# Performance work log

Hardware: AMD Instinct MI355X
Metric: run time of the kernel (lower is better)

Reference implementation:

```python
import jax, jax.numpy as jnp
import numpy as np

VIS_DIM = 768
LBL_DIM = 128
HID = 256
VIS_W = 0.4
LBL_W = 0.6
TEMP = 1.0
EPS = 1e-12  # torch F.normalize default eps


def setup_inputs() -> dict:
    key = jax.random.key(0)
    ks = jax.random.split(key, 8)
    B, N = 32, 4096
    visual_feats = jax.random.normal(ks[0], (B, N, VIS_DIM), dtype=jnp.float32)
    label_context = jax.random.normal(ks[1], (B, LBL_DIM), dtype=jnp.float32)
    visual_mask = jnp.ones((B, N), dtype=bool)
    # scorer MLP params (stored [in, out] for x @ W)
    W1 = jax.random.normal(ks[2], (VIS_DIM, HID), dtype=jnp.float32) / np.sqrt(VIS_DIM)
    b1 = jnp.zeros((HID,), dtype=jnp.float32)
    W2 = jax.random.normal(ks[3], (HID, 1), dtype=jnp.float32) / np.sqrt(HID)
    b2 = jnp.zeros((1,), dtype=jnp.float32)
    # label -> visual projection
    Wp = jax.random.normal(ks[4], (LBL_DIM, VIS_DIM), dtype=jnp.float32) / np.sqrt(LBL_DIM)
    bp = jnp.zeros((VIS_DIM,), dtype=jnp.float32)
    return {
        "visual_feats": visual_feats,
        "label_context": label_context,
        "W1": W1, "b1": b1, "W2": W2, "b2": b2, "Wp": Wp, "bp": bp,
        "visual_mask": visual_mask,
        "k": 192,
    }


def _l2norm(x):
    n = jnp.linalg.norm(x, axis=-1, keepdims=True)
    return x / jnp.maximum(n, EPS)


def reference(visual_feats, label_context, W1, b1, W2, b2, Wp, bp, visual_mask, k):
    B, N, D = visual_feats.shape
    # scoring MLP: [B,N,D] -> [B,N]
    h = jnp.maximum(jnp.einsum('bnd,dh->bnh', visual_feats, W1) + b1, 0.0)
    visual_scores = (jnp.einsum('bnh,ho->bno', h, W2) + b2)[..., 0]
    # label projection [B,D] then cosine similarity against each patch
    label_proj = label_context @ Wp + bp              # [B, D]
    vis_n = _l2norm(visual_feats)                     # [B, N, D]
    lbl_n = _l2norm(label_proj)[:, None, :]           # [B, 1, D]
    label_scores = jnp.sum(vis_n * lbl_n, axis=-1)    # [B, N]
    combined = (VIS_W * visual_scores + LBL_W * label_scores) / TEMP
    combined = jnp.where(visual_mask, combined, -jnp.inf)
    k = min(int(k), N)
    topk_scores, topk_indices = jax.lax.top_k(combined, k)   # [B, k]
    selected_feats = jnp.take_along_axis(visual_feats, topk_indices[..., None], axis=1)
    return selected_feats, topk_indices
```

## Files before the change

kernel.cpp:

```cpp
#include <hip/hip_runtime.h>
#include <hip/hip_bf16.h>

#define B_   32
#define N_   4096
#define D_   768
#define HID_ 256

#define SX 64.0f
#define SW 1024.0f
#define INV_S (1.0f / 65536.0f)

typedef unsigned long long ull;
typedef _Float16 half8 __attribute__((ext_vector_type(8)));
typedef _Float16 half4 __attribute__((ext_vector_type(4)));
typedef float f32x16 __attribute__((ext_vector_type(16)));

__device__ __forceinline__ void gload_lds16(const void* g, void* l) {
  __builtin_amdgcn_global_load_lds(
      (const __attribute__((address_space(1))) void*)g,
      (__attribute__((address_space(3))) void*)l, 16, 0, 0);
}

__global__ __launch_bounds__(256) void prep_kernel(
    const float* __restrict__ W1, _Float16* __restrict__ whi,
    _Float16* __restrict__ wlo, const float* __restrict__ lc,
    const float* __restrict__ Wp, const float* __restrict__ bp,
    float* __restrict__ lbl_n) {
  if (blockIdx.x < 96) {
    int c = blockIdx.x;
    int h = threadIdx.x;
    half8 vh, vl;
#pragma unroll
    for (int j = 0; j < 8; ++j) {
      float w = W1[(size_t)(c * 8 + j) * 256 + h] * SW;
      _Float16 hi = (_Float16)w;
      vh[j] = hi;
      vl[j] = (_Float16)(w - (float)hi);
    }
    *(half8*)&whi[((size_t)c * 256 + h) * 8] = vh;
    *(half8*)&wlo[((size_t)c * 256 + h) * 8] = vl;
    return;
  }
  int b = blockIdx.x - 96;
  int t = threadIdx.x;
  __shared__ float s_lc[128];
  __shared__ float s_out[768];
  __shared__ float s_red[4];

  if (t < 128) s_lc[t] = lc[b * 128 + t];
  __syncthreads();

  float sumsq = 0.f;
  for (int d = t; d < D_; d += 256) {
    float acc = bp[d];
    for (int k = 0; k < 128; ++k) acc += s_lc[k] * Wp[k * D_ + d];
    s_out[d] = acc;
    sumsq += acc * acc;
  }
  for (int off = 32; off >= 1; off >>= 1) sumsq += __shfl_xor(sumsq, off);
  if ((t & 63) == 0) s_red[t >> 6] = sumsq;
  __syncthreads();
  float tot = s_red[0] + s_red[1] + s_red[2] + s_red[3];
  float inv = 1.f / fmaxf(sqrtf(tot), 1e-12f);
  for (int d = t; d < D_; d += 256) lbl_n[b * D_ + d] = s_out[d] * inv;
}

__global__ __launch_bounds__(256, 3) void score12_kernel(
    const float* __restrict__ X, const _Float16* __restrict__ Whi,
    const _Float16* __restrict__ Wlo, const float* __restrict__ b1,
    const float* __restrict__ W2, const float* __restrict__ b2,
    const float* __restrict__ lbl_n, float* __restrict__ scores) {
  __shared__ __align__(16) _Float16 sWh[2][2][256][8];
  __shared__ __align__(16) _Float16 sWl[2][2][256][8];
  __shared__ __align__(16) _Float16 sB[2][2][2][64][8];
  __shared__ __align__(16) float sLbl[768];
  __shared__ float sB1[256], sW2[256];
  __shared__ float sVs[4][64];
  __shared__ float sLsc[64];

  const int t  = threadIdx.x;
  const int w  = t >> 6;
  const int l  = t & 63;
  const int l5 = l >> 5;
  const int ln = l & 31;
  const int pb = blockIdx.x * 64;
  const int batch = pb >> 12;

  const int r  = t >> 2;
  const int kq = t & 3;
  const float* xbase = X + (size_t)(pb + r) * D_ + kq * 4;

  f32x16 acc[2][2];
#pragma unroll
  for (int mt = 0; mt < 2; ++mt)
#pragma unroll
    for (int bt = 0; bt < 2; ++bt)
#pragma unroll
      for (int q = 0; q < 16; ++q) acc[mt][bt][q] = 0.f;

  float sq = 0.f, dt = 0.f;

#define GLOAD_W(S, BUF)                                                        \
  {                                                                            \
    const char* srcH = (const char*)Whi + (size_t)(S) * 8192;                  \
    const char* srcL = (const char*)Wlo + (size_t)(S) * 8192;                  \
    char* dH = (char*)&sWh[BUF][0][0][0] + w * 1024;                           \
    char* dL = (char*)&sWl[BUF][0][0][0] + w * 1024;                           \
    gload_lds16(srcH + t * 16, dH);                                            \
    gload_lds16(srcH + 4096 + t * 16, dH + 4096);                              \
    gload_lds16(srcL + t * 16, dL);                                            \
    gload_lds16(srcL + 4096 + t * 16, dL + 4096);                              \
  }

#define SPLIT_STORE(BUF, XV, SIDX)                                             \
  {                                                                            \
    half4 nh, nl;                                                              \
    const float4 lv = *(const float4*)&sLbl[(SIDX) * 16 + kq * 4];             \
    _Pragma("unroll")                                                          \
    for (int j = 0; j < 4; ++j) {                                              \
      float xv = (&(XV).x)[j];                                                 \
      sq += xv * xv;                                                           \
      dt += xv * (&lv.x)[j];                                                   \
      float xs = xv * SX;                                                      \
      _Float16 hi = (_Float16)xs;                                              \
      nh[j] = hi;                                                              \
      nl[j] = (_Float16)(xs - (float)hi);                                      \
    }                                                                          \
    *(half4*)&sB[BUF][0][kq >> 1][r][(kq & 1) * 4] = nh;                       \
    *(half4*)&sB[BUF][1][kq >> 1][r][(kq & 1) * 4] = nl;                       \
  }

  GLOAD_W(0, 0)
  float4 x0 = *(const float4*)(xbase);
  float4 xc = *(const float4*)(xbase + 16);
  for (int i = t; i < D_; i += 256) sLbl[i] = lbl_n[batch * D_ + i];
  sB1[t] = b1[t];
  sW2[t] = W2[t];
  __syncthreads();

  SPLIT_STORE(0, x0, 0)
  asm volatile("s_waitcnt lgkmcnt(0)" ::: "memory");
  __builtin_amdgcn_s_barrier();

  for (int S = 0; S < 47; ++S) {
    const int c = S & 1;
    GLOAD_W(S + 1, c ^ 1)
    const int s2 = (S + 2 > 47) ? 47 : S + 2;
    float4 xn = *(const float4*)(xbase + s2 * 16);
    __builtin_amdgcn_sched_barrier(0);

    half8 ah[2], al[2], bh[2], bl[2];
#pragma unroll
    for (int mt = 0; mt < 2; ++mt) {
      ah[mt] = *(const half8*)&sWh[c][l5][w * 64 + mt * 32 + ln][0];
      al[mt] = *(const half8*)&sWl[c][l5][w * 64 + mt * 32 + ln][0];
    }
#pragma unroll
    for (int bt = 0; bt < 2; ++bt) {
      bh[bt] = *(const half8*)&sB[c][0][l5][bt * 32 + ln][0];
      bl[bt] = *(const half8*)&sB[c][1][l5][bt * 32 + ln][0];
    }
    __builtin_amdgcn_s_setprio(1);
#pragma unroll
    for (int mt = 0; mt < 2; ++mt)
#pragma unroll
      for (int bt = 0; bt < 2; ++bt)
        acc[mt][bt] = __builtin_amdgcn_mfma_f32_32x32x16_f16(
            ah[mt], bh[bt], acc[mt][bt], 0, 0, 0);
#pragma unroll
    for (int mt = 0; mt < 2; ++mt)
#pragma unroll
      for (int bt = 0; bt < 2; ++bt)
        acc[mt][bt] = __builtin_amdgcn_mfma_f32_32x32x16_f16(
            ah[mt], bl[bt], acc[mt][bt], 0, 0, 0);
#pragma unroll
    for (int mt = 0; mt < 2; ++mt)
#pragma unroll
      for (int bt = 0; bt < 2; ++bt)
        acc[mt][bt] = __builtin_amdgcn_mfma_f32_32x32x16_f16(
            al[mt], bh[bt], acc[mt][bt], 0, 0, 0);
    __builtin_amdgcn_s_setprio(0);

    SPLIT_STORE(c ^ 1, xc, S + 1)
    xc = xn;
    asm volatile("s_waitcnt vmcnt(1) lgkmcnt(0)" ::: "memory");
    __builtin_amdgcn_sched_barrier(0);
    __builtin_amdgcn_s_barrier();
  }

  {
    half8 ah[2], al[2], bh[2], bl[2];
#pragma unroll
    for (int mt = 0; mt < 2; ++mt) {
      ah[mt] = *(const half8*)&sWh[1][l5][w * 64 + mt * 32 + ln][0];
      al[mt] = *(const half8*)&sWl[1][l5][w * 64 + mt * 32 + ln][0];
    }
#pragma unroll
    for (int bt = 0; bt < 2; ++bt) {
      bh[bt] = *(const half8*)&sB[1][0][l5][bt * 32 + ln][0];
      bl[bt] = *(const half8*)&sB[1][1][l5][bt * 32 + ln][0];
    }
#pragma unroll
    for (int mt = 0; mt < 2; ++mt)
#pragma unroll
      for (int bt = 0; bt < 2; ++bt) {
        acc[mt][bt] = __builtin_amdgcn_mfma_f32_32x32x16_f16(
            ah[mt], bh[bt], acc[mt][bt], 0, 0, 0);
      }
#pragma unroll
    for (int mt = 0; mt < 2; ++mt)
#pragma unroll
      for (int bt = 0; bt < 2; ++bt) {
        acc[mt][bt] = __builtin_amdgcn_mfma_f32_32x32x16_f16(
            ah[mt], bl[bt], acc[mt][bt], 0, 0, 0);
        acc[mt][bt] = __builtin_amdgcn_mfma_f32_32x32x16_f16(
            al[mt], bh[bt], acc[mt][bt], 0, 0, 0);
      }
  }
  __syncthreads();
#undef GLOAD_W
#undef SPLIT_STORE

  sq += __shfl_xor(sq, 1);  dt += __shfl_xor(dt, 1);
  sq += __shfl_xor(sq, 2);  dt += __shfl_xor(dt, 2);
  if ((t & 3) == 0) sLsc[r] = dt / fmaxf(sqrtf(sq), 1e-12f);

  float vsb[2] = {0.f, 0.f};
#pragma unroll
  for (int mt = 0; mt < 2; ++mt) {
#pragma unroll
    for (int rq = 0; rq < 4; ++rq) {
      const int hb = w * 64 + mt * 32 + rq * 8 + l5 * 4;
      const float4 b1v = *(const float4*)&sB1[hb];
      const float4 w2v = *(const float4*)&sW2[hb];
#pragma unroll
      for (int j = 0; j < 4; ++j) {
        float h0 = acc[mt][0][rq * 4 + j] * INV_S + (&b1v.x)[j];
        float h1 = acc[mt][1][rq * 4 + j] * INV_S + (&b1v.x)[j];
        vsb[0] += fmaxf(h0, 0.f) * (&w2v.x)[j];
        vsb[1] += fmaxf(h1, 0.f) * (&w2v.x)[j];
      }
    }
  }
  vsb[0] += __shfl_xor(vsb[0], 32);
  vsb[1] += __shfl_xor(vsb[1], 32);
  if (l < 32) {
    sVs[w][l]      = vsb[0];
    sVs[w][32 + l] = vsb[1];
  }
  __syncthreads();

  if (t < 64) {
    float vst = sVs[0][t] + sVs[1][t] + sVs[2][t] + sVs[3][t] + b2[0];
    scores[pb + t] = 0.4f * vst + 0.6f * sLsc[t];
  }
}

__global__ __launch_bounds__(256) void topk3_kernel(
    const float* __restrict__ scores, int* __restrict__ out_idx,
    float* __restrict__ out_idx_f, int K) {
  int b = blockIdx.x;
  int t = threadIdx.x;
  int wv = t >> 6, l = t & 63;
  __shared__ ull swm[4];

  ull keys[16];
#pragma unroll
  for (int j = 0; j < 16; ++j) {
    int i = (j << 8) + t;
    float s = scores[(b << 12) + i];
    unsigned u = __float_as_uint(s);
    u = (u & 0x80000000u) ? ~u : (u | 0x80000000u);
    keys[j] = ((ull)u << 32) | (unsigned)(4095 - i);
  }
  ull cur = 0;
#pragma unroll
  for (int j = 0; j < 16; ++j) cur = keys[j] > cur ? keys[j] : cur;

  {
    ull wb = cur;
#pragma unroll
    for (int off = 1; off < 64; off <<= 1) {
      ull o = __shfl_xor(wb, off);
      wb = o > wb ? o : wb;
    }
    if (l == 0) swm[wv] = wb;
  }
  __syncthreads();

  for (int sel = 0; sel < K; ++sel) {
    ull m0 = swm[0] > swm[1] ? swm[0] : swm[1];
    ull m1 = swm[2] > swm[3] ? swm[2] : swm[3];
    ull best = m0 > m1 ? m0 : m1;
    if (t == 0) {
      int id = 4095 - (int)(unsigned)(best & 0xFFFFFFFFull);
      out_idx[b * K + sel] = id;
      out_idx_f[b * K + sel] = (float)id;
    }
    if (swm[wv] == best) {
      if (cur == best) {
        cur = 0;
#pragma unroll
        for (int j = 0; j < 16; ++j)
          cur = (keys[j] < best && keys[j] > cur) ? keys[j] : cur;
      }
      ull wb = cur;
#pragma unroll
      for (int off = 1; off < 64; off <<= 1) {
        ull o = __shfl_xor(wb, off);
        wb = o > wb ? o : wb;
      }
      if (l == 0) swm[wv] = wb;
    }
    __syncthreads();
  }
}

__global__ __launch_bounds__(192) void gather_kernel(
    const float* __restrict__ feats, const int* __restrict__ idx,
    float* __restrict__ out_feats, int K) {
  int i = blockIdx.x;
  int b = blockIdx.y;
  int id = idx[b * K + i];
  const float4* src = (const float4*)&feats[((size_t)b * N_ + id) * D_];
  float4* dst = (float4*)&out_feats[((size_t)b * K + i) * D_];
  dst[threadIdx.x] = src[threadIdx.x];
}

extern "C" void kernel_launch(void* const* d_in, const int* in_sizes, int n_in,
                              void* d_out, int out_size, void* d_ws, size_t ws_size,
                              hipStream_t stream) {
  const float* feats = (const float*)d_in[0];
  const float* lc    = (const float*)d_in[1];
  const float* W1    = (const float*)d_in[2];
  const float* b1    = (const float*)d_in[3];
  const float* W2    = (const float*)d_in[4];
  const float* b2    = (const float*)d_in[5];
  const float* Wp    = (const float*)d_in[6];
  const float* bp    = (const float*)d_in[7];
  int K = out_size / (B_ * (D_ + 1));

  float* ws_f    = (float*)d_ws;
  float* lbl_n   = ws_f;
  float* scoresv = ws_f + B_ * D_;
  int*   topidx  = (int*)(ws_f + B_ * D_ + B_ * N_);
  size_t off = (size_t)B_ * D_ + (size_t)B_ * N_ + B_ * 256;
  off = (off + 3) & ~(size_t)3;
  _Float16* whi = (_Float16*)(ws_f + off);
  _Float16* wlo = whi + (size_t)96 * 256 * 8;

  float* out_f     = (float*)d_out;
  float* out_idx_f = out_f + (size_t)B_ * K * D_;

  prep_kernel<<<128, 256, 0, stream>>>(W1, whi, wlo, lc, Wp, bp, lbl_n);
  score12_kernel<<<(B_ * N_) / 64, 256, 0, stream>>>(feats, whi, wlo, b1, W2, b2,
                                                     lbl_n, scoresv);
  topk3_kernel<<<B_, 256, 0, stream>>>(scoresv, topidx, out_idx_f, K);
  gather_kernel<<<dim3(K, B_), 192, 0, stream>>>(feats, topidx, out_f, K);
}
```

Before: 371.9 us.

## Keep W1 fragments in registers with triple-buffered prefetch, 128-patch blocks

The scoring kernel now uses 512-thread blocks covering 128 patches. Each wave handles one 64-wide hidden slice and one 64-patch half. W1 hi/lo fragments are no longer staged through LDS: they are loaded straight from global memory into registers with a three-deep rotating prefetch, and the main loop is unrolled into six-phase groups. This drops the LDS traffic and footprint for weights and doubles the patch tile. In exchange it costs more registers, and each wave issues more global weight loads, which lean on L2.

```diff
diff --git a/kernel.cpp b/kernel.cpp
--- a/kernel.cpp
+++ b/kernel.cpp
@@ -14,12 +14,6 @@
 typedef _Float16 half8 __attribute__((ext_vector_type(8)));
 typedef _Float16 half4 __attribute__((ext_vector_type(4)));
 typedef float f32x16 __attribute__((ext_vector_type(16)));
-
-__device__ __forceinline__ void gload_lds16(const void* g, void* l) {
-  __builtin_amdgcn_global_load_lds(
-      (const __attribute__((address_space(1))) void*)g,
-      (__attribute__((address_space(3))) void*)l, 16, 0, 0);
-}
 
 __global__ __launch_bounds__(256) void prep_kernel(
     const float* __restrict__ W1, _Float16* __restrict__ whi,
@@ -65,31 +59,35 @@
   for (int d = t; d < D_; d += 256) lbl_n[b * D_ + d] = s_out[d] * inv;
 }
 
-__global__ __launch_bounds__(256, 3) void score12_kernel(
+__global__ __launch_bounds__(512, 2) void score13_kernel(
     const float* __restrict__ X, const _Float16* __restrict__ Whi,
     const _Float16* __restrict__ Wlo, const float* __restrict__ b1,
     const float* __restrict__ W2, const float* __restrict__ b2,
     const float* __restrict__ lbl_n, float* __restrict__ scores) {
-  __shared__ __align__(16) _Float16 sWh[2][2][256][8];
-  __shared__ __align__(16) _Float16 sWl[2][2][256][8];
-  __shared__ __align__(16) _Float16 sB[2][2][2][64][8];
+  __shared__ __align__(16) _Float16 sB[2][2][2][128][8];
   __shared__ __align__(16) float sLbl[768];
   __shared__ float sB1[256], sW2[256];
-  __shared__ float sVs[4][64];
-  __shared__ float sLsc[64];
+  __shared__ float sVs[4][128];
+  __shared__ float sLsc[128];
 
   const int t  = threadIdx.x;
   const int w  = t >> 6;
   const int l  = t & 63;
   const int l5 = l >> 5;
   const int ln = l & 31;
-  const int pb = blockIdx.x * 64;
+  const int hh = w >> 1;
+  const int pg = w & 1;
+  const int pb = blockIdx.x * 128;
   const int batch = pb >> 12;
 
   const int r  = t >> 2;
   const int kq = t & 3;
   const float* xbase = X + (size_t)(pb + r) * D_ + kq * 4;
 
+  const half8* gWh = (const half8*)Whi;
+  const half8* gWl = (const half8*)Wlo;
+  const int hidb = hh * 64 + ln;
+
   f32x16 acc[2][2];
 #pragma unroll
   for (int mt = 0; mt < 2; ++mt)
@@ -99,20 +97,10 @@
       for (int q = 0; q < 16; ++q) acc[mt][bt][q] = 0.f;
 
   float sq = 0.f, dt = 0.f;
-
-#define GLOAD_W(S, BUF)                                                        \
-  {                                                                            \
-    const char* srcH = (const char*)Whi + (size_t)(S) * 8192;                  \
-    const char* srcL = (const char*)Wlo + (size_t)(S) * 8192;                  \
-    char* dH = (char*)&sWh[BUF][0][0][0] + w * 1024;                           \
-    char* dL = (char*)&sWl[BUF][0][0][0] + w * 1024;                           \
-    gload_lds16(srcH + t * 16, dH);                                            \
-    gload_lds16(srcH + 4096 + t * 16, dH + 4096);                              \
-    gload_lds16(srcL + t * 16, dL);                                            \
-    gload_lds16(srcL + 4096 + t * 16, dL + 4096);                              \
-  }
-
-#define SPLIT_STORE(BUF, XV, SIDX)                                             \
+  half8 wH[3][2], wL[3][2];
+  float4 xr[2];
+
+#define SPLIT(TB, XV, SIDX)                                                    \
   {                                                                            \
     half4 nh, nl;                                                              \
     const float4 lv = *(const float4*)&sLbl[(SIDX) * 16 + kq * 4];             \
@@ -126,100 +114,84 @@
       nh[j] = hi;                                                              \
       nl[j] = (_Float16)(xs - (float)hi);                                      \
     }                                                                          \
-    *(half4*)&sB[BUF][0][kq >> 1][r][(kq & 1) * 4] = nh;                       \
-    *(half4*)&sB[BUF][1][kq >> 1][r][(kq & 1) * 4] = nl;                       \
-  }
-
-  GLOAD_W(0, 0)
-  float4 x0 = *(const float4*)(xbase);
-  float4 xc = *(const float4*)(xbase + 16);
-  for (int i = t; i < D_; i += 256) sLbl[i] = lbl_n[batch * D_ + i];
-  sB1[t] = b1[t];
-  sW2[t] = W2[t];
-  __syncthreads();
-
-  SPLIT_STORE(0, x0, 0)
+    *(half4*)&sB[TB][0][kq >> 1][r][(kq & 1) * 4] = nh;                        \
+    *(half4*)&sB[TB][1][kq >> 1][r][(kq & 1) * 4] = nl;                        \
+  }
+
+#define PHASE(S, CSET, PSET, CBUF)                                             \
+  {                                                                            \
+    const int S_ = (S);                                                        \
+       \
+    {                                                                          \
+      const int sw = (S_ + 2 > 47) ? 47 : S_ + 2;                              \
+      const int cc = sw * 2 + l5;                                              \
+      wH[PSET][0] = gWh[cc * 256 + hidb];                                      \
+      wH[PSET][1] = gWh[cc * 256 + hidb + 32];                                 \
+      wL[PSET][0] = gWl[cc * 256 + hidb];                                      \
+      wL[PSET][1] = gWl[cc * 256 + hidb + 32];                                 \
+    }                                                                          \
+                                    \
+    {                                                                          \
+      const int sx = (S_ + 2 > 47) ? 47 : S_ + 2;                              \
+      xr[CBUF] = *(const float4*)(xbase + sx * 16);                            \
+    }                                                                          \
+                                                       \
+    half8 bh0 = *(const half8*)&sB[CBUF][0][l5][pg * 64 + ln][0];              \
+    half8 bl0 = *(const half8*)&sB[CBUF][1][l5][pg * 64 + ln][0];              \
+    half8 bh1 = *(const half8*)&sB[CBUF][0][l5][pg * 64 + 32 + ln][0];         \
+    half8 bl1 = *(const half8*)&sB[CBUF][1][l5][pg * 64 + 32 + ln][0];         \
+    __builtin_amdgcn_sched_barrier(0);                                         \
+        \
+    asm volatile("s_waitcnt vmcnt(5)" ::: "memory");                           \
+    __builtin_amdgcn_sched_barrier(0);                                         \
+    if (S_ < 47) { SPLIT((CBUF) ^ 1, xr[(CBUF) ^ 1], S_ + 1) }                 \
+    asm volatile("s_waitcnt lgkmcnt(0)" ::: "memory");                         \
+    __builtin_amdgcn_sched_barrier(0);                                         \
+    __builtin_amdgcn_s_barrier();                                              \
+                                           \
+    __builtin_amdgcn_s_setprio(1);                                             \
+    acc[0][0] = __builtin_amdgcn_mfma_f32_32x32x16_f16(wH[CSET][0], bh0, acc[0][0], 0, 0, 0); \
+    acc[1][0] = __builtin_amdgcn_mfma_f32_32x32x16_f16(wH[CSET][1], bh0, acc[1][0], 0, 0, 0); \
+    acc[0][1] = __builtin_amdgcn_mfma_f32_32x32x16_f16(wH[CSET][0], bh1, acc[0][1], 0, 0, 0); \
+    acc[1][1] = __builtin_amdgcn_mfma_f32_32x32x16_f16(wH[CSET][1], bh1, acc[1][1], 0, 0, 0); \
+    acc[0][0] = __builtin_amdgcn_mfma_f32_32x32x16_f16(wH[CSET][0], bl0, acc[0][0], 0, 0, 0); \
+    acc[1][0] = __builtin_amdgcn_mfma_f32_32x32x16_f16(wH[CSET][1], bl0, acc[1][0], 0, 0, 0); \
+    acc[0][1] = __builtin_amdgcn_mfma_f32_32x32x16_f16(wH[CSET][0], bl1, acc[0][1], 0, 0, 0); \
+    acc[1][1] = __builtin_amdgcn_mfma_f32_32x32x16_f16(wH[CSET][1], bl1, acc[1][1], 0, 0, 0); \
+    acc[0][0] = __builtin_amdgcn_mfma_f32_32x32x16_f16(wL[CSET][0], bh0, acc[0][0], 0, 0, 0); \
+    acc[1][0] = __builtin_amdgcn_mfma_f32_32x32x16_f16(wL[CSET][1], bh0, acc[1][0], 0, 0, 0); \
+    acc[0][1] = __builtin_amdgcn_mfma_f32_32x32x16_f16(wL[CSET][0], bh1, acc[0][1], 0, 0, 0); \
+    acc[1][1] = __builtin_amdgcn_mfma_f32_32x32x16_f16(wL[CSET][1], bh1, acc[1][1], 0, 0, 0); \
+    __builtin_amdgcn_s_setprio(0);                                             \
+  }
+
+  for (int i = t; i < D_; i += 512) sLbl[i] = lbl_n[batch * D_ + i];
+  if (t < 256) { sB1[t] = b1[t]; sW2[t] = W2[t]; }
+  {
+    wH[0][0] = gWh[l5 * 256 + hidb];        wH[0][1] = gWh[l5 * 256 + hidb + 32];
+    wL[0][0] = gWl[l5 * 256 + hidb];        wL[0][1] = gWl[l5 * 256 + hidb + 32];
+    const int c1 = 2 + l5;
+    wH[1][0] = gWh[c1 * 256 + hidb];        wH[1][1] = gWh[c1 * 256 + hidb + 32];
+    wL[1][0] = gWl[c1 * 256 + hidb];        wL[1][1] = gWl[c1 * 256 + hidb + 32];
+  }
+  xr[0] = *(const float4*)(xbase);
+  xr[1] = *(const float4*)(xbase + 16);
+  __syncthreads();
+
+  SPLIT(0, xr[0], 0)
   asm volatile("s_waitcnt lgkmcnt(0)" ::: "memory");
   __builtin_amdgcn_s_barrier();
 
-  for (int S = 0; S < 47; ++S) {
-    const int c = S & 1;
-    GLOAD_W(S + 1, c ^ 1)
-    const int s2 = (S + 2 > 47) ? 47 : S + 2;
-    float4 xn = *(const float4*)(xbase + s2 * 16);
-    __builtin_amdgcn_sched_barrier(0);
-
-    half8 ah[2], al[2], bh[2], bl[2];
-#pragma unroll
-    for (int mt = 0; mt < 2; ++mt) {
-      ah[mt] = *(const half8*)&sWh[c][l5][w * 64 + mt * 32 + ln][0];
-      al[mt] = *(const half8*)&sWl[c][l5][w * 64 + mt * 32 + ln][0];
-    }
-#pragma unroll
-    for (int bt = 0; bt < 2; ++bt) {
-      bh[bt] = *(const half8*)&sB[c][0][l5][bt * 32 + ln][0];
-      bl[bt] = *(const half8*)&sB[c][1][l5][bt * 32 + ln][0];
-    }
-    __builtin_amdgcn_s_setprio(1);
-#pragma unroll
-    for (int mt = 0; mt < 2; ++mt)
-#pragma unroll
-      for (int bt = 0; bt < 2; ++bt)
-        acc[mt][bt] = __builtin_amdgcn_mfma_f32_32x32x16_f16(
-            ah[mt], bh[bt], acc[mt][bt], 0, 0, 0);
-#pragma unroll
-    for (int mt = 0; mt < 2; ++mt)
-#pragma unroll
-      for (int bt = 0; bt < 2; ++bt)
-        acc[mt][bt] = __builtin_amdgcn_mfma_f32_32x32x16_f16(
-            ah[mt], bl[bt], acc[mt][bt], 0, 0, 0);
-#pragma unroll
-    for (int mt = 0; mt < 2; ++mt)
-#pragma unroll
-      for (int bt = 0; bt < 2; ++bt)
-        acc[mt][bt] = __builtin_amdgcn_mfma_f32_32x32x16_f16(
-            al[mt], bh[bt], acc[mt][bt], 0, 0, 0);
-    __builtin_amdgcn_s_setprio(0);
-
-    SPLIT_STORE(c ^ 1, xc, S + 1)
-    xc = xn;
-    asm volatile("s_waitcnt vmcnt(1) lgkmcnt(0)" ::: "memory");
-    __builtin_amdgcn_sched_barrier(0);
-    __builtin_amdgcn_s_barrier();
-  }
-
-  {
-    half8 ah[2], al[2], bh[2], bl[2];
-#pragma unroll
-    for (int mt = 0; mt < 2; ++mt) {
-      ah[mt] = *(const half8*)&sWh[1][l5][w * 64 + mt * 32 + ln][0];
-      al[mt] = *(const half8*)&sWl[1][l5][w * 64 + mt * 32 + ln][0];
-    }
-#pragma unroll
-    for (int bt = 0; bt < 2; ++bt) {
-      bh[bt] = *(const half8*)&sB[1][0][l5][bt * 32 + ln][0];
-      bl[bt] = *(const half8*)&sB[1][1][l5][bt * 32 + ln][0];
-    }
-#pragma unroll
-    for (int mt = 0; mt < 2; ++mt)
-#pragma unroll
-      for (int bt = 0; bt < 2; ++bt) {
-        acc[mt][bt] = __builtin_amdgcn_mfma_f32_32x32x16_f16(
-            ah[mt], bh[bt], acc[mt][bt], 0, 0, 0);
-      }
-#pragma unroll
-    for (int mt = 0; mt < 2; ++mt)
-#pragma unroll
-      for (int bt = 0; bt < 2; ++bt) {
-        acc[mt][bt] = __builtin_amdgcn_mfma_f32_32x32x16_f16(
-            ah[mt], bl[bt], acc[mt][bt], 0, 0, 0);
-        acc[mt][bt] = __builtin_amdgcn_mfma_f32_32x32x16_f16(
-            al[mt], bh[bt], acc[mt][bt], 0, 0, 0);
-      }
-  }
-  __syncthreads();
-#undef GLOAD_W
-#undef SPLIT_STORE
+  for (int s6 = 0; s6 < 48; s6 += 6) {
+    PHASE(s6 + 0, 0, 2, 0)
+    PHASE(s6 + 1, 1, 0, 1)
+    PHASE(s6 + 2, 2, 1, 0)
+    PHASE(s6 + 3, 0, 2, 1)
+    PHASE(s6 + 4, 1, 0, 0)
+    PHASE(s6 + 5, 2, 1, 1)
+  }
+#undef PHASE
+#undef SPLIT
 
   sq += __shfl_xor(sq, 1);  dt += __shfl_xor(dt, 1);
   sq += __shfl_xor(sq, 2);  dt += __shfl_xor(dt, 2);
@@ -230,7 +202,7 @@
   for (int mt = 0; mt < 2; ++mt) {
 #pragma unroll
     for (int rq = 0; rq < 4; ++rq) {
-      const int hb = w * 64 + mt * 32 + rq * 8 + l5 * 4;
+      const int hb = hh * 64 + mt * 32 + rq * 8 + l5 * 4;
       const float4 b1v = *(const float4*)&sB1[hb];
       const float4 w2v = *(const float4*)&sW2[hb];
 #pragma unroll
@@ -245,12 +217,12 @@
   vsb[0] += __shfl_xor(vsb[0], 32);
   vsb[1] += __shfl_xor(vsb[1], 32);
   if (l < 32) {
-    sVs[w][l]      = vsb[0];
-    sVs[w][32 + l] = vsb[1];
-  }
-  __syncthreads();
-
-  if (t < 64) {
+    sVs[hh][pg * 64 + l]      = vsb[0];
+    sVs[hh][pg * 64 + 32 + l] = vsb[1];
+  }
+  __syncthreads();
+
+  if (t < 128) {
     float vst = sVs[0][t] + sVs[1][t] + sVs[2][t] + sVs[3][t] + b2[0];
     scores[pb + t] = 0.4f * vst + 0.6f * sLsc[t];
   }
@@ -353,8 +325,8 @@
   float* out_idx_f = out_f + (size_t)B_ * K * D_;
 
   prep_kernel<<<128, 256, 0, stream>>>(W1, whi, wlo, lc, Wp, bp, lbl_n);
-  score12_kernel<<<(B_ * N_) / 64, 256, 0, stream>>>(feats, whi, wlo, b1, W2, b2,
-                                                     lbl_n, scoresv);
+  score13_kernel<<<(B_ * N_) / 128, 512, 0, stream>>>(feats, whi, wlo, b1, W2, b2,
+                                                      lbl_n, scoresv);
   topk3_kernel<<<B_, 256, 0, stream>>>(scoresv, topidx, out_idx_f, K);
   gather_kernel<<<dim3(K, B_), 192, 0, stream>>>(feats, topidx, out_f, K);
 }
```

Result: slower. 393.6 us (+5.9%).
